# Kernel tuning notes

Hardware: AMD Instinct MI355X
Metric: run time of the kernel (lower is better)

Reference implementation:

```python
import jax, jax.numpy as jnp
import numpy as np

D_MODEL = 1024
NUM_HEADS = 16
D_K = D_MODEL // NUM_HEADS


def setup_inputs() -> dict:
    key = jax.random.key(0)
    ks = jax.random.split(key, 9)
    s = 1.0 / np.sqrt(D_MODEL)
    return {
        "z": jax.random.normal(ks[0], (4, 2048, D_MODEL), dtype=jnp.float32),
        "Wq": jax.random.uniform(ks[1], (D_MODEL, D_MODEL), jnp.float32, -s, s),
        "bq": jax.random.uniform(ks[2], (D_MODEL,), jnp.float32, -s, s),
        "Wk": jax.random.uniform(ks[3], (D_MODEL, D_MODEL), jnp.float32, -s, s),
        "bk": jax.random.uniform(ks[4], (D_MODEL,), jnp.float32, -s, s),
        "Wv": jax.random.uniform(ks[5], (D_MODEL, D_MODEL), jnp.float32, -s, s),
        "bv": jax.random.uniform(ks[6], (D_MODEL,), jnp.float32, -s, s),
        "Wo": jax.random.uniform(ks[7], (D_MODEL, D_MODEL), jnp.float32, -s, s),
        "bo": jax.random.uniform(ks[8], (D_MODEL,), jnp.float32, -s, s),
    }


def reference(z, Wq, bq, Wk, bk, Wv, bv, Wo, bo):
    B, S, _ = z.shape
    # project and split heads: [B, H, S, d_k]
    def proj(W, b):
        return (z @ W.T + b).reshape(B, S, NUM_HEADS, D_K).transpose(0, 2, 1, 3)
    Q, K, V = proj(Wq, bq), proj(Wk, bk), proj(Wv, bv)
    scale = 1.0 / np.sqrt(D_K)
    scores = jnp.einsum('bhqd,bhkd->bhqk', Q, K) * scale
    probs = jax.nn.softmax(scores, axis=-1)
    ctx = jnp.einsum('bhqk,bhkd->bhqd', probs, V)
    ctx = ctx.transpose(0, 2, 1, 3).reshape(B, S, D_MODEL)
    return ctx @ Wo.T + bo
```

## Files before the change

### kernel.cpp

```cpp
#include <hip/hip_runtime.h>
#include <stdint.h>

#define D_MODEL 1024
#define NHEAD 16
#define DKH 64
#define BATCH 4
#define SEQ 2048
#define M_ROWS (BATCH*SEQ)
#define NBH (BATCH*NHEAD)

typedef float f32x4 __attribute__((ext_vector_type(4)));
typedef float f32x16 __attribute__((ext_vector_type(16)));
typedef __bf16 bf16x8 __attribute__((ext_vector_type(8)));
typedef short short4v __attribute__((ext_vector_type(4)));
typedef unsigned short ushort4v __attribute__((ext_vector_type(4)));
typedef unsigned short ushort8v __attribute__((ext_vector_type(8)));
typedef int int2v __attribute__((ext_vector_type(2)));
typedef int int4v __attribute__((ext_vector_type(4)));

__device__ __forceinline__ unsigned short f2bf(float x) {
    __bf16 b = (__bf16)x;
    return __builtin_bit_cast(unsigned short, b);
}
__device__ __forceinline__ unsigned int packbf2(float lo, float hi) {
    return (unsigned int)f2bf(lo) | ((unsigned int)f2bf(hi) << 16);
}

#define GLL(gsrc, ldst) \
    __builtin_amdgcn_global_load_lds((const __attribute__((address_space(1))) void*)(gsrc), \
                                     (__attribute__((address_space(3))) void*)(ldst), 16, 0, 0)


__device__ __forceinline__ void cvt8store(const float* __restrict__ src,
                                          unsigned short* __restrict__ dst) {
    float4 v0 = *(const float4*)(src);
    float4 v1 = *(const float4*)(src + 4);
    ushort8v o;
    o[0] = f2bf(v0.x); o[1] = f2bf(v0.y); o[2] = f2bf(v0.z); o[3] = f2bf(v0.w);
    o[4] = f2bf(v1.x); o[5] = f2bf(v1.y); o[6] = f2bf(v1.z); o[7] = f2bf(v1.w);
    *(ushort8v*)dst = o;
}

__global__ __launch_bounds__(256) void k_convert(
    const float* __restrict__ z,  const float* __restrict__ wq,
    const float* __restrict__ wk, const float* __restrict__ wv,
    const float* __restrict__ wo,
    const float* __restrict__ bq, const float* __restrict__ bk,
    const float* __restrict__ bv,
    unsigned short* __restrict__ zf, unsigned short* __restrict__ wqkvf,
    unsigned short* __restrict__ wobf, float* __restrict__ biasf)
{
    int i = blockIdx.x * 256 + threadIdx.x;
    if (i < 1048576) {
        int lane = i & 63, rest = i >> 6;
        int kk = rest & 1, mfrag = (rest >> 1) & 7, half = (rest >> 4) & 1;
        int kt = (rest >> 5) & 15, mtile = rest >> 9;
        int row = mtile * 256 + half * 128 + mfrag * 16 + (lane & 15);
        int k = kt * 64 + kk * 32 + (lane >> 4) * 8;
        cvt8store(z + (size_t)row * 1024 + k, zf + (size_t)i * 8);
    }
    int i2 = i - 1048576;
    if (i2 >= 0 && i2 < 393216) {
        int lane = i2 & 63, rest = i2 >> 6;
        int kk = rest & 1, nfrag = (rest >> 1) & 7;
        int kt = (rest >> 4) & 15, ntile = rest >> 8;
        int n = ntile * 128 + nfrag * 16 + (lane & 15);
        int k = kt * 64 + kk * 32 + (lane >> 4) * 8;
        const float* W = (n < 1024) ? wq : ((n < 2048) ? wk : wv);
        cvt8store(W + (size_t)(n & 1023) * 1024 + k, wqkvf + (size_t)i2 * 8);
    }
    int i3 = i2 - 393216;
    if (i3 >= 0 && i3 < 131072) {
        int lane = i3 & 63, rest = i3 >> 6;
        int kk = rest & 1, nfrag = (rest >> 1) & 7;
        int kt = (rest >> 4) & 15, ntile = rest >> 8;
        int n = ntile * 128 + nfrag * 16 + (lane & 15);
        int k = kt * 64 + kk * 32 + (lane >> 4) * 8;
        cvt8store(wo + (size_t)n * 1024 + k, wobf + (size_t)i3 * 8);
    }
    if (i < 1024) {
        biasf[i]        = bq[i];
        biasf[1024 + i] = bk[i];
        biasf[2048 + i] = bv[i];
    }
}

__device__ __forceinline__ void g_stage(const unsigned short* __restrict__ as_,
                                        const unsigned short* __restrict__ bs_,
                                        unsigned short* la, unsigned short* lb,
                                        int wid, int lane)
{
#pragma unroll
    for (int g = 0; g < 4; ++g)
        GLL(as_ + (wid + 8 * g) * 512 + lane * 8, la + (wid + 8 * g) * 512);
#pragma unroll
    for (int g = 0; g < 2; ++g)
        GLL(bs_ + (wid + 8 * g) * 512 + lane * 8, lb + (wid + 8 * g) * 512);
}

#define GEMM_KLOOP(Abase, Bbase)                                                      \
    g_stage(Abase, Bbase, &ldsA[0][0], &ldsB[0][0], wid, lane);                       \
    g_stage(Abase + 16384, Bbase + 8192, &ldsA[1][0], &ldsB[1][0], wid, lane);        \
    asm volatile("s_waitcnt vmcnt(6)" ::: "memory");                                  \
    __builtin_amdgcn_s_barrier();                                                     \
    for (int t = 0; t < 16; ++t) {                                                    \
        int buf = t % 3;                                                              \
        if (t + 2 < 16)                                                               \
            g_stage(Abase + (size_t)(t + 2) * 16384, Bbase + (size_t)(t + 2) * 8192,  \
                    &ldsA[(t + 2) % 3][0], &ldsB[(t + 2) % 3][0], wid, lane);         \
        const unsigned short* A = &ldsA[buf][0];                                      \
        const unsigned short* B = &ldsB[buf][0];                                      \
        bf16x8 b00 = *(const bf16x8*)(B + ((wn * 2 + 0) * 2 + 0) * 512 + lane * 8);   \
        bf16x8 b01 = *(const bf16x8*)(B + ((wn * 2 + 0) * 2 + 1) * 512 + lane * 8);   \
        bf16x8 b10 = *(const bf16x8*)(B + ((wn * 2 + 1) * 2 + 0) * 512 + lane * 8);   \
        bf16x8 b11 = *(const bf16x8*)(B + ((wn * 2 + 1) * 2 + 1) * 512 + lane * 8);   \
        _Pragma("unroll")                                                             \
        for (int ii = 0; ii < 8; ++ii) {                                              \
            bf16x8 a0 = *(const bf16x8*)(A + ((wm * 8 + ii) * 2 + 0) * 512 + lane * 8); \
            bf16x8 a1 = *(const bf16x8*)(A + ((wm * 8 + ii) * 2 + 1) * 512 + lane * 8); \
            acc[ii][0] = __builtin_amdgcn_mfma_f32_16x16x32_bf16(a0, b00, acc[ii][0], 0, 0, 0); \
            acc[ii][0] = __builtin_amdgcn_mfma_f32_16x16x32_bf16(a1, b01, acc[ii][0], 0, 0, 0); \
            acc[ii][1] = __builtin_amdgcn_mfma_f32_16x16x32_bf16(a0, b10, acc[ii][1], 0, 0, 0); \
            acc[ii][1] = __builtin_amdgcn_mfma_f32_16x16x32_bf16(a1, b11, acc[ii][1], 0, 0, 0); \
        }                                                                             \
        if (t < 14)       { asm volatile("s_waitcnt vmcnt(6)" ::: "memory"); }        \
        else if (t == 14) { asm volatile("s_waitcnt vmcnt(0)" ::: "memory"); }        \
        if (t < 15) { __builtin_amdgcn_sched_barrier(0); __builtin_amdgcn_s_barrier(); } \
    }

__global__ __launch_bounds__(512) void k_gemm_qkv(
    const unsigned short* __restrict__ Af,
    const unsigned short* __restrict__ Bf,
    const float* __restrict__ biasf,
    unsigned short* __restrict__ qb, unsigned short* __restrict__ kfrag,
    unsigned short* __restrict__ vfrag)
{
    __shared__ unsigned short ldsA[3][16384];
    __shared__ unsigned short ldsB[3][8192];

    int bid = blockIdx.x;
    int wg = (bid & 7) * 96 + (bid >> 3);
    int tn = wg % 24, tm = wg / 24;
    int tid = threadIdx.x, wid = tid >> 6, lane = tid & 63;
    int wm = wid >> 2, wn = wid & 3;

    const unsigned short* Abase = Af + (size_t)tm * 16 * 16384;
    const unsigned short* Bbase = Bf + (size_t)tn * 16 * 8192;

    f32x4 acc[8][2] = {};
    GEMM_KLOOP(Abase, Bbase)

    const float QSC = 0.18033688011112042f;
    int t3 = tn >> 3;
#pragma unroll
    for (int j = 0; j < 2; ++j) {
        int col = tn * 128 + wn * 32 + j * 16 + (lane & 15);
        float bias = biasf[col];
        int d = col & 1023, h = d >> 6, dk = d & 63;
#pragma unroll
        for (int i = 0; i < 8; ++i) {
#pragma unroll
            for (int r = 0; r < 4; ++r) {
                int row = tm * 256 + wm * 128 + i * 16 + (lane >> 4) * 4 + r;
                float v = acc[i][j][r] + bias;
                if (t3 == 0) v *= QSC;
                unsigned short bv16 = f2bf(v);
                int b_ = row >> 11, s_ = row & 2047;
                int bh = b_ * NHEAD + h;
                if (t3 == 0) {
                    qb[((size_t)bh * SEQ + s_) * DKH + dk] = bv16;
                } else if (t3 == 1) {
                    int kvblk = s_ >> 6, r64 = s_ & 63;
                    int t32 = r64 >> 5, l5 = r64 & 31;
                    int ds = dk >> 4, hi2 = (dk >> 3) & 1, e = dk & 7;
                    kfrag[((size_t)(bh * 32 + kvblk)) * 4096 +
                          (t32 * 4 + ds) * 512 + (hi2 * 32 + l5) * 8 + e] = bv16;
                } else {
                    int kvblk = s_ >> 6, kv64 = s_ & 63;
                    int s16 = kv64 >> 4, hi2 = (kv64 >> 3) & 1, e = kv64 & 7;
                    int vt = dk >> 5, l5 = dk & 31;
                    vfrag[((size_t)(bh * 32 + kvblk)) * 4096 +
                          (vt * 4 + s16) * 512 + (hi2 * 32 + l5) * 8 + e] = bv16;
                }
            }
        }
    }
}

__global__ __launch_bounds__(512) void k_attn(
    const unsigned short* __restrict__ qg,
    const unsigned short* __restrict__ kb,
    const unsigned short* __restrict__ vtb,
    unsigned short* __restrict__ ctxf)
{
    int bid = blockIdx.x;
    int x = bid & 7, li = bid >> 3;
    int bh = x * 8 + (li >> 3);
    int qt = li & 7;

    int tid = threadIdx.x, wid = tid >> 6, lane = tid & 63;
    int lq = lane & 31, hi = lane >> 5;

    bf16x8 aq[4];
    {
        const unsigned short* qp = qg + ((size_t)bh * SEQ + qt * 256 + wid * 32 + lq) * DKH + hi * 8;
#pragma unroll
        for (int d = 0; d < 4; ++d) aq[d] = *(const bf16x8*)(qp + d * 16);
    }

    float lsum = 0.f;
    f32x16 oa0 = {};
    f32x16 oa1 = {};

    const unsigned short* kp = kb  + (size_t)bh * 32 * 4096 + lane * 8;
    const unsigned short* vp = vtb + (size_t)bh * 32 * 4096 + lane * 8;

    for (int kt = 0; kt < 32; ++kt) {
        bf16x8 kf[8];
#pragma unroll
        for (int f = 0; f < 8; ++f) kf[f] = *(const bf16x8*)(kp + f * 512);

        f32x16 st0 = {}, st1 = {};
        __builtin_amdgcn_s_setprio(1);
#pragma unroll
        for (int ds = 0; ds < 4; ++ds) {
            st0 = __builtin_amdgcn_mfma_f32_32x32x16_bf16(kf[ds],     aq[ds], st0, 0, 0, 0);
            st1 = __builtin_amdgcn_mfma_f32_32x32x16_bf16(kf[4 + ds], aq[ds], st1, 0, 0, 0);
        }
        __builtin_amdgcn_s_setprio(0);

        bf16x8 vf[8];
#pragma unroll
        for (int f = 0; f < 8; ++f) vf[f] = *(const bf16x8*)(vp + f * 512);

        unsigned int w16[16];
#pragma unroll
        for (int jj = 0; jj < 8; ++jj) {
            float p0 = __builtin_amdgcn_exp2f(st0[2 * jj]);
            float p1 = __builtin_amdgcn_exp2f(st0[2 * jj + 1]);
            lsum += p0 + p1;
            w16[jj] = packbf2(p0, p1);
        }
#pragma unroll
        for (int jj = 0; jj < 8; ++jj) {
            float p0 = __builtin_amdgcn_exp2f(st1[2 * jj]);
            float p1 = __builtin_amdgcn_exp2f(st1[2 * jj + 1]);
            lsum += p0 + p1;
            w16[8 + jj] = packbf2(p0, p1);
        }
        bf16x8 w[4];
#pragma unroll
        for (int s = 0; s < 4; ++s) {
            int base = (s >> 1) * 8 + (s & 1) * 4;
            int2v r1 = __builtin_amdgcn_permlane32_swap((int)w16[base + 0], (int)w16[base + 2], false, false);
            int2v r2 = __builtin_amdgcn_permlane32_swap((int)w16[base + 1], (int)w16[base + 3], false, false);
            int4v fr; fr[0] = r1[0]; fr[1] = r2[0]; fr[2] = r1[1]; fr[3] = r2[1];
            w[s] = __builtin_bit_cast(bf16x8, fr);
        }

        __builtin_amdgcn_s_setprio(1);
#pragma unroll
        for (int s = 0; s < 4; ++s) {
            oa0 = __builtin_amdgcn_mfma_f32_32x32x16_bf16(vf[s],     w[s], oa0, 0, 0, 0);
            oa1 = __builtin_amdgcn_mfma_f32_32x32x16_bf16(vf[4 + s], w[s], oa1, 0, 0, 0);
        }
        __builtin_amdgcn_s_setprio(0);

        kp += 4096; vp += 4096;
    }

    int b_ = bh >> 4, h = bh & 15;
    lsum += __shfl_xor(lsum, 32);
    float inv = 1.0f / lsum;
    int s_ = qt * 256 + wid * 32 + lq;
    int row = b_ * 2048 + s_;
    int mtile = row >> 8, half = (row >> 7) & 1, mfrag = (row >> 4) & 7, lrow = row & 15;
    unsigned short* cb = ctxf + (size_t)((mtile * 16 + h) * 2 + half) * 8192
                              + mfrag * 1024 + lrow * 8 + 4 * hi;
#pragma unroll
    for (int m = 0; m < 4; ++m) {
        ushort4v s0, s1;
        s0[0] = f2bf(oa0[4 * m + 0] * inv); s0[1] = f2bf(oa0[4 * m + 1] * inv);
        s0[2] = f2bf(oa0[4 * m + 2] * inv); s0[3] = f2bf(oa0[4 * m + 3] * inv);
        *(ushort4v*)(cb + m * 128) = s0;
        s1[0] = f2bf(oa1[4 * m + 0] * inv); s1[1] = f2bf(oa1[4 * m + 1] * inv);
        s1[2] = f2bf(oa1[4 * m + 2] * inv); s1[3] = f2bf(oa1[4 * m + 3] * inv);
        *(ushort4v*)(cb + 512 + m * 128) = s1;
    }
}

__global__ __launch_bounds__(512) void k_gemm_out(
    const unsigned short* __restrict__ Af,
    const unsigned short* __restrict__ Bf,
    const float* __restrict__ bo,
    float* __restrict__ out)
{
    __shared__ unsigned short ldsA[3][16384];
    __shared__ unsigned short ldsB[3][8192];

    int bid = blockIdx.x;
    int wg = (bid & 7) * 32 + (bid >> 3);
    int tn = wg % 8, tm = wg / 8;
    int tid = threadIdx.x, wid = tid >> 6, lane = tid & 63;
    int wm = wid >> 2, wn = wid & 3;

    const unsigned short* Abase = Af + (size_t)tm * 16 * 16384;
    const unsigned short* Bbase = Bf + (size_t)tn * 16 * 8192;

    f32x4 acc[8][2] = {};
    GEMM_KLOOP(Abase, Bbase)

#pragma unroll
    for (int j = 0; j < 2; ++j) {
        int col = tn * 128 + wn * 32 + j * 16 + (lane & 15);
        float bias = bo[col];
#pragma unroll
        for (int i = 0; i < 8; ++i) {
#pragma unroll
            for (int r = 0; r < 4; ++r) {
                int row = tm * 256 + wm * 128 + i * 16 + (lane >> 4) * 4 + r;
                out[(size_t)row * 1024 + col] = acc[i][j][r] + bias;
            }
        }
    }
}

extern "C" void kernel_launch(void* const* d_in, const int* in_sizes, int n_in,
                              void* d_out, int out_size, void* d_ws, size_t ws_size,
                              hipStream_t stream)
{
    const float* z  = (const float*)d_in[0];
    const float* Wq = (const float*)d_in[1];
    const float* bq = (const float*)d_in[2];
    const float* Wk = (const float*)d_in[3];
    const float* bk = (const float*)d_in[4];
    const float* Wv = (const float*)d_in[5];
    const float* bv = (const float*)d_in[6];
    const float* Wo = (const float*)d_in[7];
    const float* bo = (const float*)d_in[8];
    float* out = (float*)d_out;

    char* ws = (char*)d_ws;
    unsigned short* zf    = (unsigned short*)(ws);
    unsigned short* ctxf  = (unsigned short*)(ws);
    unsigned short* wqkvf = (unsigned short*)(ws + (16ull << 20));
    unsigned short* wobf  = (unsigned short*)(ws + (22ull << 20));
    float*          biasf = (float*)(ws + (24ull << 20));
    unsigned short* qb    = (unsigned short*)(ws + (25ull << 20));
    unsigned short* kfrag = (unsigned short*)(ws + (41ull << 20));
    unsigned short* vfrag = (unsigned short*)(ws + (57ull << 20));

    k_convert<<<8192, 256, 0, stream>>>(z, Wq, Wk, Wv, Wo, bq, bk, bv, zf, wqkvf, wobf, biasf);
    k_gemm_qkv<<<768, 512, 0, stream>>>(zf, wqkvf, biasf, qb, kfrag, vfrag);
    k_attn<<<NBH * 8, 512, 0, stream>>>(qb, kfrag, vfrag, ctxf);
    k_gemm_out<<<256, 512, 0, stream>>>(ctxf, wobf, bo, out);
}
```

Baseline: 209.6 us.

## Switch GEMMs to 32x32x16 MFMA with matching fragment layouts

```diff
diff --git a/kernel.cpp b/kernel.cpp
--- a/kernel.cpp
+++ b/kernel.cpp
@@ -12,7 +12,6 @@
 typedef float f32x4 __attribute__((ext_vector_type(4)));
 typedef float f32x16 __attribute__((ext_vector_type(16)));
 typedef __bf16 bf16x8 __attribute__((ext_vector_type(8)));
-typedef short short4v __attribute__((ext_vector_type(4)));
 typedef unsigned short ushort4v __attribute__((ext_vector_type(4)));
 typedef unsigned short ushort8v __attribute__((ext_vector_type(8)));
 typedef int int2v __attribute__((ext_vector_type(2)));
@@ -53,29 +52,29 @@
     int i = blockIdx.x * 256 + threadIdx.x;
     if (i < 1048576) {
         int lane = i & 63, rest = i >> 6;
-        int kk = rest & 1, mfrag = (rest >> 1) & 7, half = (rest >> 4) & 1;
+        int kk16 = rest & 3, mf32 = (rest >> 2) & 7;
         int kt = (rest >> 5) & 15, mtile = rest >> 9;
-        int row = mtile * 256 + half * 128 + mfrag * 16 + (lane & 15);
-        int k = kt * 64 + kk * 32 + (lane >> 4) * 8;
+        int row = mtile * 256 + mf32 * 32 + (lane & 31);
+        int k = kt * 64 + kk16 * 16 + (lane >> 5) * 8;
         cvt8store(z + (size_t)row * 1024 + k, zf + (size_t)i * 8);
     }
     int i2 = i - 1048576;
     if (i2 >= 0 && i2 < 393216) {
         int lane = i2 & 63, rest = i2 >> 6;
-        int kk = rest & 1, nfrag = (rest >> 1) & 7;
+        int kk16 = rest & 3, nf32 = (rest >> 2) & 3;
         int kt = (rest >> 4) & 15, ntile = rest >> 8;
-        int n = ntile * 128 + nfrag * 16 + (lane & 15);
-        int k = kt * 64 + kk * 32 + (lane >> 4) * 8;
+        int n = ntile * 128 + nf32 * 32 + (lane & 31);
+        int k = kt * 64 + kk16 * 16 + (lane >> 5) * 8;
         const float* W = (n < 1024) ? wq : ((n < 2048) ? wk : wv);
         cvt8store(W + (size_t)(n & 1023) * 1024 + k, wqkvf + (size_t)i2 * 8);
     }
     int i3 = i2 - 393216;
     if (i3 >= 0 && i3 < 131072) {
         int lane = i3 & 63, rest = i3 >> 6;
-        int kk = rest & 1, nfrag = (rest >> 1) & 7;
+        int kk16 = rest & 3, nf32 = (rest >> 2) & 3;
         int kt = (rest >> 4) & 15, ntile = rest >> 8;
-        int n = ntile * 128 + nfrag * 16 + (lane & 15);
-        int k = kt * 64 + kk * 32 + (lane >> 4) * 8;
+        int n = ntile * 128 + nf32 * 32 + (lane & 31);
+        int k = kt * 64 + kk16 * 16 + (lane >> 5) * 8;
         cvt8store(wo + (size_t)n * 1024 + k, wobf + (size_t)i3 * 8);
     }
     if (i < 1024) {
@@ -110,18 +109,16 @@
                     &ldsA[(t + 2) % 3][0], &ldsB[(t + 2) % 3][0], wid, lane);         \
         const unsigned short* A = &ldsA[buf][0];                                      \
         const unsigned short* B = &ldsB[buf][0];                                      \
-        bf16x8 b00 = *(const bf16x8*)(B + ((wn * 2 + 0) * 2 + 0) * 512 + lane * 8);   \
-        bf16x8 b01 = *(const bf16x8*)(B + ((wn * 2 + 0) * 2 + 1) * 512 + lane * 8);   \
-        bf16x8 b10 = *(const bf16x8*)(B + ((wn * 2 + 1) * 2 + 0) * 512 + lane * 8);   \
-        bf16x8 b11 = *(const bf16x8*)(B + ((wn * 2 + 1) * 2 + 1) * 512 + lane * 8);   \
         _Pragma("unroll")                                                             \
-        for (int ii = 0; ii < 8; ++ii) {                                              \
-            bf16x8 a0 = *(const bf16x8*)(A + ((wm * 8 + ii) * 2 + 0) * 512 + lane * 8); \
-            bf16x8 a1 = *(const bf16x8*)(A + ((wm * 8 + ii) * 2 + 1) * 512 + lane * 8); \
-            acc[ii][0] = __builtin_amdgcn_mfma_f32_16x16x32_bf16(a0, b00, acc[ii][0], 0, 0, 0); \
-            acc[ii][0] = __builtin_amdgcn_mfma_f32_16x16x32_bf16(a1, b01, acc[ii][0], 0, 0, 0); \
-            acc[ii][1] = __builtin_amdgcn_mfma_f32_16x16x32_bf16(a0, b10, acc[ii][1], 0, 0, 0); \
-            acc[ii][1] = __builtin_amdgcn_mfma_f32_16x16x32_bf16(a1, b11, acc[ii][1], 0, 0, 0); \
+        for (int kk = 0; kk < 4; ++kk) {                                              \
+            bf16x8 a0 = *(const bf16x8*)(A + ((2 * wm + 0) * 4 + kk) * 512 + lane * 8); \
+            bf16x8 a1 = *(const bf16x8*)(A + ((2 * wm + 1) * 4 + kk) * 512 + lane * 8); \
+            bf16x8 b0 = *(const bf16x8*)(B + ((2 * wn + 0) * 4 + kk) * 512 + lane * 8); \
+            bf16x8 b1 = *(const bf16x8*)(B + ((2 * wn + 1) * 4 + kk) * 512 + lane * 8); \
+            acc[0][0] = __builtin_amdgcn_mfma_f32_32x32x16_bf16(a0, b0, acc[0][0], 0, 0, 0); \
+            acc[0][1] = __builtin_amdgcn_mfma_f32_32x32x16_bf16(a0, b1, acc[0][1], 0, 0, 0); \
+            acc[1][0] = __builtin_amdgcn_mfma_f32_32x32x16_bf16(a1, b0, acc[1][0], 0, 0, 0); \
+            acc[1][1] = __builtin_amdgcn_mfma_f32_32x32x16_bf16(a1, b1, acc[1][1], 0, 0, 0); \
         }                                                                             \
         if (t < 14)       { asm volatile("s_waitcnt vmcnt(6)" ::: "memory"); }        \
         else if (t == 14) { asm volatile("s_waitcnt vmcnt(0)" ::: "memory"); }        \
@@ -142,27 +139,28 @@
     int wg = (bid & 7) * 96 + (bid >> 3);
     int tn = wg % 24, tm = wg / 24;
     int tid = threadIdx.x, wid = tid >> 6, lane = tid & 63;
-    int wm = wid >> 2, wn = wid & 3;
+    int wm = wid >> 1, wn = wid & 1;
 
     const unsigned short* Abase = Af + (size_t)tm * 16 * 16384;
     const unsigned short* Bbase = Bf + (size_t)tn * 16 * 8192;
 
-    f32x4 acc[8][2] = {};
+    f32x16 acc[2][2] = {};
     GEMM_KLOOP(Abase, Bbase)
 
     const float QSC = 0.18033688011112042f;
     int t3 = tn >> 3;
-#pragma unroll
-    for (int j = 0; j < 2; ++j) {
-        int col = tn * 128 + wn * 32 + j * 16 + (lane & 15);
+    int rowc = (lane >> 5) * 4;
+#pragma unroll
+    for (int bn = 0; bn < 2; ++bn) {
+        int col = tn * 128 + wn * 64 + bn * 32 + (lane & 31);
         float bias = biasf[col];
         int d = col & 1023, h = d >> 6, dk = d & 63;
 #pragma unroll
-        for (int i = 0; i < 8; ++i) {
-#pragma unroll
-            for (int r = 0; r < 4; ++r) {
-                int row = tm * 256 + wm * 128 + i * 16 + (lane >> 4) * 4 + r;
-                float v = acc[i][j][r] + bias;
+        for (int am = 0; am < 2; ++am) {
+#pragma unroll
+            for (int r = 0; r < 16; ++r) {
+                int row = tm * 256 + wm * 64 + am * 32 + (r & 3) + 8 * (r >> 2) + rowc;
+                float v = acc[am][bn][r] + bias;
                 if (t3 == 0) v *= QSC;
                 unsigned short bv16 = f2bf(v);
                 int b_ = row >> 11, s_ = row & 2047;
@@ -274,18 +272,19 @@
     float inv = 1.0f / lsum;
     int s_ = qt * 256 + wid * 32 + lq;
     int row = b_ * 2048 + s_;
-    int mtile = row >> 8, half = (row >> 7) & 1, mfrag = (row >> 4) & 7, lrow = row & 15;
-    unsigned short* cb = ctxf + (size_t)((mtile * 16 + h) * 2 + half) * 8192
-                              + mfrag * 1024 + lrow * 8 + 4 * hi;
-#pragma unroll
-    for (int m = 0; m < 4; ++m) {
+    int mtile = row >> 8, mf32 = (row >> 5) & 7;
+    unsigned short* cb = ctxf + ((size_t)((mtile * 16 + h) * 8 + mf32)) * 2048 + 4 * hi;
+#pragma unroll
+    for (int g = 0; g < 4; ++g) {
+        int off0 = (2 * 0 + (g >> 1)) * 512 + (lq + 32 * (g & 1)) * 8;
+        int off1 = (2 * 1 + (g >> 1)) * 512 + (lq + 32 * (g & 1)) * 8;
         ushort4v s0, s1;
-        s0[0] = f2bf(oa0[4 * m + 0] * inv); s0[1] = f2bf(oa0[4 * m + 1] * inv);
-        s0[2] = f2bf(oa0[4 * m + 2] * inv); s0[3] = f2bf(oa0[4 * m + 3] * inv);
-        *(ushort4v*)(cb + m * 128) = s0;
-        s1[0] = f2bf(oa1[4 * m + 0] * inv); s1[1] = f2bf(oa1[4 * m + 1] * inv);
-        s1[2] = f2bf(oa1[4 * m + 2] * inv); s1[3] = f2bf(oa1[4 * m + 3] * inv);
-        *(ushort4v*)(cb + 512 + m * 128) = s1;
+        s0[0] = f2bf(oa0[4 * g + 0] * inv); s0[1] = f2bf(oa0[4 * g + 1] * inv);
+        s0[2] = f2bf(oa0[4 * g + 2] * inv); s0[3] = f2bf(oa0[4 * g + 3] * inv);
+        *(ushort4v*)(cb + off0) = s0;
+        s1[0] = f2bf(oa1[4 * g + 0] * inv); s1[1] = f2bf(oa1[4 * g + 1] * inv);
+        s1[2] = f2bf(oa1[4 * g + 2] * inv); s1[3] = f2bf(oa1[4 * g + 3] * inv);
+        *(ushort4v*)(cb + off1) = s1;
     }
 }
 
@@ -302,24 +301,25 @@
     int wg = (bid & 7) * 32 + (bid >> 3);
     int tn = wg % 8, tm = wg / 8;
     int tid = threadIdx.x, wid = tid >> 6, lane = tid & 63;
-    int wm = wid >> 2, wn = wid & 3;
+    int wm = wid >> 1, wn = wid & 1;
 
     const unsigned short* Abase = Af + (size_t)tm * 16 * 16384;
     const unsigned short* Bbase = Bf + (size_t)tn * 16 * 8192;
 
-    f32x4 acc[8][2] = {};
+    f32x16 acc[2][2] = {};
     GEMM_KLOOP(Abase, Bbase)
 
-#pragma unroll
-    for (int j = 0; j < 2; ++j) {
-        int col = tn * 128 + wn * 32 + j * 16 + (lane & 15);
+    int rowc = (lane >> 5) * 4;
+#pragma unroll
+    for (int bn = 0; bn < 2; ++bn) {
+        int col = tn * 128 + wn * 64 + bn * 32 + (lane & 31);
         float bias = bo[col];
 #pragma unroll
-        for (int i = 0; i < 8; ++i) {
-#pragma unroll
-            for (int r = 0; r < 4; ++r) {
-                int row = tm * 256 + wm * 128 + i * 16 + (lane >> 4) * 4 + r;
-                out[(size_t)row * 1024 + col] = acc[i][j][r] + bias;
+        for (int am = 0; am < 2; ++am) {
+#pragma unroll
+            for (int r = 0; r < 16; ++r) {
+                int row = tm * 256 + wm * 64 + am * 32 + (r & 3) + 8 * (r >> 2) + rowc;
+                out[(size_t)row * 1024 + col] = acc[am][bn][r] + bias;
             }
         }
     }
```

After: 207.8 us. Within noise of the previous version (-0.8%).
